# Kernel optimization log

Hardware: AMD Instinct MI355X
Metric: run time of the kernel (lower is better)

## Reference

```python
import jax, jax.numpy as jnp
import numpy as np

B, S, D = 2, 2048, 1024
H = 16
DK = D // H  # 64


def _rope_tables():
    # standard RoPE frequencies, shaped (1,1,S,DK//2) for clean broadcasting
    half = DK // 2
    inv_freq = 1.0 / (10000.0 ** (np.arange(0, half, dtype=np.float32) * 2.0 / DK))
    t = np.arange(S, dtype=np.float32)
    ang = np.einsum('s,d->sd', t, inv_freq)  # (S, half)
    sin = jnp.asarray(np.sin(ang))[None, None]  # (1,1,S,half)
    cos = jnp.asarray(np.cos(ang))[None, None]
    return sin, cos


def setup_inputs() -> dict:
    key = jax.random.key(0)
    ks = jax.random.split(key, 12)
    scale = 1.0 / np.sqrt(D)
    k = jax.random.normal(ks[0], (B, S, D), jnp.float32)
    q = jax.random.normal(ks[1], (B, S, D), jnp.float32)
    v = jax.random.normal(ks[2], (B, S, D), jnp.float32)
    # causal mask, broadcast over batch and heads: (1,1,S,S)
    mask = jnp.tril(jnp.ones((S, S), jnp.int32))[None, None]
    sin, cos = _rope_tables()
    Wk = jax.random.normal(ks[3], (D, D), jnp.float32) * scale
    bk = jax.random.normal(ks[4], (D,), jnp.float32) * scale
    Wq = jax.random.normal(ks[5], (D, D), jnp.float32) * scale
    bq = jax.random.normal(ks[6], (D,), jnp.float32) * scale
    Wv = jax.random.normal(ks[7], (D, D), jnp.float32) * scale
    bv = jax.random.normal(ks[8], (D,), jnp.float32) * scale
    Wo = jax.random.normal(ks[9], (D, D), jnp.float32) * scale
    bo = jax.random.normal(ks[10], (D,), jnp.float32) * scale
    return dict(k=k, q=q, v=v, mask=mask, sin=sin, cos=cos,
                Wk=Wk, bk=bk, Wq=Wq, bq=bq, Wv=Wv, bv=bv, Wo=Wo, bo=bo)


def _apply_rope(x, sin, cos):
    # x: (B,H,S,DK); sin/cos: (1,1,S,DK//2)
    x1 = x[..., ::2]
    x2 = x[..., 1::2]
    even = x1 * cos - x2 * sin
    odd = x1 * sin + x2 * cos
    return jnp.stack((even, odd), axis=-1).reshape(x.shape)


def reference(k, q, v, mask, sin, cos, Wk, bk, Wq, bq, Wv, bv, Wo, bo):
    # projections (nn.Linear: x @ W.T + b)
    def proj(x, W, b):
        y = x @ W.T + b
        return y.reshape(B, S, H, DK).transpose(0, 2, 1, 3)  # (B,H,S,DK)

    key = proj(k, Wk, bk)
    query = proj(q, Wq, bq)
    value = proj(v, Wv, bv)

    query = _apply_rope(query, sin, cos)
    key = _apply_rope(key, sin, cos)

    scores = jnp.einsum('bhqd,bhkd->bhqk', query, key) / jnp.sqrt(jnp.float32(DK))
    scores = jnp.where(mask == 0, jnp.float32(-1e9), scores)
    attn = jax.nn.softmax(scores, axis=-1)  # dropout=0 -> identity
    x = jnp.einsum('bhqk,bhkd->bhqd', attn, value)
    x = x.transpose(0, 2, 1, 3).reshape(B, S, D)
    return x @ Wo.T + bo
```

## Files before the change

### kernel.cpp

```cpp
#include <hip/hip_runtime.h>
#include <hip/hip_bf16.h>

typedef __bf16 bf16x8 __attribute__((ext_vector_type(8)));
typedef __bf16 bf16x4 __attribute__((ext_vector_type(4)));
typedef float  f32x4  __attribute__((ext_vector_type(4)));

static constexpr int B = 2, S = 2048, D = 1024, H = 16, DK = 64;
static constexpr int M = B * S;
static constexpr int NE = M * D;
static constexpr int WE = D * D;

__device__ inline float fast_exp2(float x) { return __builtin_amdgcn_exp2f(x); }

__device__ inline void gload16(const void* g, void* l) {
  __builtin_amdgcn_global_load_lds(
      (const __attribute__((address_space(1))) void*)g,
      (__attribute__((address_space(3))) void*)l, 16, 0, 0);
}

__device__ inline int perm64(int i) {
  return (((i >> 2) & 3) << 4) | (((i >> 5) & 1) << 3) | (((i >> 4) & 1) << 2) | (i & 3);
}

__global__ __launch_bounds__(256) void cvt_all(
    const float* __restrict__ q, const float* __restrict__ k,
    const float* __restrict__ v, const float* __restrict__ Wq,
    const float* __restrict__ Wk, const float* __restrict__ Wv,
    const float* __restrict__ Wo,
    __bf16* __restrict__ Xq, __bf16* __restrict__ Xk,
    __bf16* __restrict__ Xv, __bf16* __restrict__ Wall)
{
  int z = blockIdx.y;
  const float* src; __bf16* dst; int n4;
  switch (z) {
    case 0: src = q;  dst = Xq;            n4 = NE / 4; break;
    case 1: src = k;  dst = Xk;            n4 = NE / 4; break;
    case 2: src = v;  dst = Xv;            n4 = NE / 4; break;
    case 3: src = Wq; dst = Wall;          n4 = WE / 4; break;
    case 4: src = Wk; dst = Wall + WE;     n4 = WE / 4; break;
    case 5: src = Wv; dst = Wall + 2*WE;   n4 = WE / 4; break;
    default:src = Wo; dst = Wall + 3*WE;   n4 = WE / 4; break;
  }
  int i = blockIdx.x * blockDim.x + threadIdx.x;
  int stride = gridDim.x * blockDim.x;
  for (; i < n4; i += stride) {
    float4 f = reinterpret_cast<const float4*>(src)[i];
    bf16x4 o;
    o[0] = (__bf16)f.x; o[1] = (__bf16)f.y; o[2] = (__bf16)f.z; o[3] = (__bf16)f.w;
    reinterpret_cast<bf16x4*>(dst)[i] = o;
  }
}

__global__ __launch_bounds__(256) void proj_kernel(
    const __bf16* __restrict__ Xq, const __bf16* __restrict__ Xk,
    const __bf16* __restrict__ Xv, const __bf16* __restrict__ Wall,
    const float* __restrict__ bq_, const float* __restrict__ bk_,
    const float* __restrict__ bv_,
    const float* __restrict__ sinp, const float* __restrict__ cosp,
    __bf16* __restrict__ Qr, __bf16* __restrict__ Kr, __bf16* __restrict__ Vt)
{
  __shared__ __align__(16) __bf16 As[128 * 32];
  __shared__ __align__(16) __bf16 Bs[128 * 32];
  int tid = threadIdx.x;
  int lane = tid & 63, wid = tid >> 6;
  int lr = lane & 15, lg = lane >> 4;
  int wr = wid >> 1, wc = wid & 1;
  int m0 = blockIdx.x * 128;
  int by = blockIdx.y;
  int z  = by >> 3;
  const __bf16* A    = (z == 0) ? Xq : (z == 1) ? Xk : Xv;
  const __bf16* Bw   = Wall + (size_t)by * 128 * 1024;
  const float*  bias = (z == 0) ? bq_ : (z == 1) ? bk_ : bv_;

  int off0 = tid * 16;
  int row0 = off0 >> 6;
  int ce0  = (off0 & 63) >> 1;
  char* asw = (char*)As + wid * 1024;
  char* bsw = (char*)Bs + wid * 1024;

  f32x4 acc[4][4];
#pragma unroll
  for (int i = 0; i < 4; ++i)
#pragma unroll
    for (int j = 0; j < 4; ++j) acc[i][j] = (f32x4){0, 0, 0, 0};

  for (int k0 = 0; k0 < 1024; k0 += 32) {
    gload16(A  + (size_t)(m0 + row0)      * 1024 + k0 + ce0, asw);
    gload16(A  + (size_t)(m0 + row0 + 64) * 1024 + k0 + ce0, asw + 4096);
    gload16(Bw + (size_t)(row0)           * 1024 + k0 + ce0, bsw);
    gload16(Bw + (size_t)(row0 + 64)      * 1024 + k0 + ce0, bsw + 4096);
    __syncthreads();
    bf16x8 af[4], bf[4];
#pragma unroll
    for (int mi = 0; mi < 4; ++mi)
      af[mi] = *reinterpret_cast<const bf16x8*>(&As[(wr*64 + mi*16 + lr)*32 + lg*8]);
#pragma unroll
    for (int ni = 0; ni < 4; ++ni)
      bf[ni] = *reinterpret_cast<const bf16x8*>(&Bs[(wc*64 + ni*16 + lr)*32 + lg*8]);
#pragma unroll
    for (int mi = 0; mi < 4; ++mi)
#pragma unroll
      for (int ni = 0; ni < 4; ++ni)
        acc[mi][ni] = __builtin_amdgcn_mfma_f32_16x16x32_bf16(af[mi], bf[ni], acc[mi][ni], 0, 0, 0);
    __syncthreads();
  }

#pragma unroll
  for (int ni = 0; ni < 4; ++ni) {
    int cf  = by * 128 + wc * 64 + ni * 16 + lr;
    int col = cf & 1023;
    int h = col >> 6, dk = col & 63, tt = dk >> 1;
    float bval = bias[col];
#pragma unroll
    for (int mi = 0; mi < 4; ++mi) {
#pragma unroll
      for (int i = 0; i < 4; ++i) {
        int r = m0 + wr * 64 + mi * 16 + lg * 4 + i;
        int s = r & (S - 1), bb = r >> 11;
        float val = acc[mi][ni][i] + bval;
        if (z < 2) {
          float part = __shfl_xor(val, 1);
          float sn = sinp[s * 32 + tt], cs = cosp[s * 32 + tt];
          float ov = (dk & 1) ? (part * sn + val * cs) : (val * cs - part * sn);
          if (z == 0) ov *= 0.18033688011112042f;
          __bf16* dst = (z == 0) ? Qr : Kr;
          dst[((size_t)(bb * H + h) * S + s) * DK + dk] = (__bf16)ov;
        } else {
          int sp = (s & ~63) | perm64(s & 63);
          Vt[((size_t)(bb * H + h) * DK + dk) * S + sp] = (__bf16)val;
        }
      }
    }
  }
}

__global__ __launch_bounds__(256) void outproj_kernel(
    const __bf16* __restrict__ AO, const __bf16* __restrict__ Wo,
    const float* __restrict__ bo_, float* __restrict__ out)
{
  __shared__ __align__(16) __bf16 As[128 * 32];
  __shared__ __align__(16) __bf16 Bs[128 * 32];
  int tid = threadIdx.x;
  int lane = tid & 63, wid = tid >> 6;
  int lr = lane & 15, lg = lane >> 4;
  int wr = wid >> 1, wc = wid & 1;
  int m0 = blockIdx.x * 128;
  int n0 = blockIdx.y * 128;

  int off0 = tid * 16;
  int row0 = off0 >> 6;
  int ce0  = (off0 & 63) >> 1;
  char* asw = (char*)As + wid * 1024;
  char* bsw = (char*)Bs + wid * 1024;

  f32x4 acc[4][4];
#pragma unroll
  for (int i = 0; i < 4; ++i)
#pragma unroll
    for (int j = 0; j < 4; ++j) acc[i][j] = (f32x4){0, 0, 0, 0};

  for (int k0 = 0; k0 < 1024; k0 += 32) {
    gload16(AO + (size_t)(m0 + row0)      * 1024 + k0 + ce0, asw);
    gload16(AO + (size_t)(m0 + row0 + 64) * 1024 + k0 + ce0, asw + 4096);
    gload16(Wo + (size_t)(n0 + row0)      * 1024 + k0 + ce0, bsw);
    gload16(Wo + (size_t)(n0 + row0 + 64) * 1024 + k0 + ce0, bsw + 4096);
    __syncthreads();
    bf16x8 af[4], bf[4];
#pragma unroll
    for (int mi = 0; mi < 4; ++mi)
      af[mi] = *reinterpret_cast<const bf16x8*>(&As[(wr*64 + mi*16 + lr)*32 + lg*8]);
#pragma unroll
    for (int ni = 0; ni < 4; ++ni)
      bf[ni] = *reinterpret_cast<const bf16x8*>(&Bs[(wc*64 + ni*16 + lr)*32 + lg*8]);
#pragma unroll
    for (int mi = 0; mi < 4; ++mi)
#pragma unroll
      for (int ni = 0; ni < 4; ++ni)
        acc[mi][ni] = __builtin_amdgcn_mfma_f32_16x16x32_bf16(af[mi], bf[ni], acc[mi][ni], 0, 0, 0);
    __syncthreads();
  }

#pragma unroll
  for (int ni = 0; ni < 4; ++ni) {
    int c = n0 + wc * 64 + ni * 16 + lr;
    float bval = bo_[c];
#pragma unroll
    for (int mi = 0; mi < 4; ++mi)
#pragma unroll
      for (int i = 0; i < 4; ++i) {
        int r = m0 + wr * 64 + mi * 16 + lg * 4 + i;
        out[(size_t)r * 1024 + c] = acc[mi][ni][i] + bval;
      }
  }
}

__global__ __launch_bounds__(256, 4) void attn_kernel(
    const __bf16* __restrict__ Qr, const __bf16* __restrict__ Kr,
    const __bf16* __restrict__ Vt, __bf16* __restrict__ AO)
{
  __shared__ __align__(16) char smem[32768];
  int tid = threadIdx.x;
  int lane = tid & 63, wid = tid >> 6;
  int lr = lane & 15, lg = lane >> 4;
  int bx = blockIdx.x;
  int bh = (bx & 7) * 4 + ((bx >> 3) & 3);
  int qb = 31 - (bx >> 5);
  int q0 = qb * 64 + wid * 16;
  int nsteps = qb + 1;

  const char* Kb = (const char*)(Kr + (size_t)bh * S * DK);
  const char* Vb = (const char*)(Vt + (size_t)bh * DK * S);
  const __bf16* Qh = Qr + (size_t)bh * S * DK;

  int o_lo = wid * 1024 + lane * 16;
#define STAGE(sel, kv0)                                                        \
  {                                                                            \
    char* kdst = smem + (sel) * 16384;                                         \
    _Pragma("unroll")                                                          \
    for (int i = 0; i < 2; ++i) {                                              \
      int o = o_lo + i * 4096;                                                 \
      int row = o >> 7;                                                        \
      int colp = (o & 127) ^ ((row & 7) << 4);                                 \
      gload16(Kb + (((size_t)((kv0) + row)) << 7) + colp,                      \
              kdst + wid * 1024 + i * 4096);                                   \
      gload16(Vb + ((size_t)row * S + (kv0)) * 2 + colp,                       \
              kdst + 8192 + wid * 1024 + i * 4096);                            \
    }                                                                          \
  }

  bf16x8 bq[2];
#pragma unroll
  for (int kc = 0; kc < 2; ++kc)
    bq[kc] = *(const bf16x8*)(Qh + (size_t)(q0 + lr) * DK + kc * 32 + lg * 8);

  int swz = (lr & 7) << 4;
  int oK0 = lr * 128 + ((lg * 16) ^ swz);
  int oK1 = lr * 128 + ((64 + lg * 16) ^ swz);
  int oV0 = lr * 128 + ((lg * 32) ^ swz);
  int oV1 = lr * 128 + ((16 + lg * 32) ^ swz);

  f32x4 o[4];
  float m2 = -3e38f, l2 = 0.f;
#pragma unroll
  for (int dt = 0; dt < 4; ++dt) o[dt] = (f32x4){0, 0, 0, 0};

  STAGE(0, 0);
  __syncthreads();

  for (int j = 0; j < nsteps; ++j) {
    int sel = j & 1;
    if (j + 1 < nsteps) STAGE(sel ^ 1, (j + 1) * 64);
    const char* kbuf = smem + sel * 16384;
    const char* vbuf = kbuf + 8192;
    int kv0 = j * 64;

    f32x4 sc[4];
#pragma unroll
    for (int kt = 0; kt < 4; ++kt) {
      bf16x8 ka0 = *(const bf16x8*)(kbuf + oK0 + kt * 2048);
      bf16x8 ka1 = *(const bf16x8*)(kbuf + oK1 + kt * 2048);
      f32x4 s = (f32x4){0, 0, 0, 0};
      s = __builtin_amdgcn_mfma_f32_16x16x32_bf16(ka0, bq[0], s, 0, 0, 0);
      s = __builtin_amdgcn_mfma_f32_16x16x32_bf16(ka1, bq[1], s, 0, 0, 0);
      sc[kt] = s;
    }

    if (j == qb) {
#pragma unroll
      for (int kt = 0; kt < 4; ++kt)
#pragma unroll
        for (int i = 0; i < 4; ++i)
          if (kv0 + kt * 16 + lg * 4 + i > q0 + lr)
            sc[kt][i] = -3e38f;
    }

    float tm = fmaxf(
        fmaxf(fmaxf(fmaxf(sc[0][0], sc[0][1]), fmaxf(sc[0][2], sc[0][3])),
              fmaxf(fmaxf(sc[1][0], sc[1][1]), fmaxf(sc[1][2], sc[1][3]))),
        fmaxf(fmaxf(fmaxf(sc[2][0], sc[2][1]), fmaxf(sc[2][2], sc[2][3])),
              fmaxf(fmaxf(sc[3][0], sc[3][1]), fmaxf(sc[3][2], sc[3][3]))));
    tm = fmaxf(tm, __shfl_xor(tm, 16));
    tm = fmaxf(tm, __shfl_xor(tm, 32));
    if (__any(tm > m2 + 8.0f)) {
      float mn = fmaxf(m2, tm);
      float f = fast_exp2(m2 - mn);
      m2 = mn;
      l2 *= f;
#pragma unroll
      for (int dt = 0; dt < 4; ++dt) o[dt] *= f;
    }
    float p[16];
#pragma unroll
    for (int kt = 0; kt < 4; ++kt)
#pragma unroll
      for (int i = 0; i < 4; ++i)
        p[kt * 4 + i] = fast_exp2(sc[kt][i] - m2);
    float sum = (((p[0] + p[1]) + (p[2] + p[3])) + ((p[4] + p[5]) + (p[6] + p[7]))) +
                (((p[8] + p[9]) + (p[10] + p[11])) + ((p[12] + p[13]) + (p[14] + p[15])));
    sum += __shfl_xor(sum, 16);
    sum += __shfl_xor(sum, 32);
    l2 += sum;
    bf16x8 pb[2];
#pragma unroll
    for (int kc = 0; kc < 2; ++kc) {
      bf16x8 pv;
#pragma unroll
      for (int a = 0; a < 2; ++a)
#pragma unroll
        for (int r = 0; r < 4; ++r)
          pv[a * 4 + r] = (__bf16)p[(2 * kc + a) * 4 + r];
      pb[kc] = pv;
    }

#pragma unroll
    for (int dt = 0; dt < 4; ++dt) {
      bf16x8 v0 = *(const bf16x8*)(vbuf + oV0 + dt * 2048);
      bf16x8 v1 = *(const bf16x8*)(vbuf + oV1 + dt * 2048);
      o[dt] = __builtin_amdgcn_mfma_f32_16x16x32_bf16(v0, pb[0], o[dt], 0, 0, 0);
      o[dt] = __builtin_amdgcn_mfma_f32_16x16x32_bf16(v1, pb[1], o[dt], 0, 0, 0);
    }
    __syncthreads();
  }
#undef STAGE

  int b = bh >> 4, h = bh & 15;
  float inv = 1.f / l2;
  int s = q0 + lr;
#pragma unroll
  for (int dt = 0; dt < 4; ++dt) {
    bf16x4 w;
#pragma unroll
    for (int i = 0; i < 4; ++i) w[i] = (__bf16)(o[dt][i] * inv);
    *(bf16x4*)&AO[(((size_t)(b * S + s)) * H + h) * DK + dt * 16 + lg * 4] = w;
  }
}

extern "C" void kernel_launch(void* const* d_in, const int* in_sizes, int n_in,
                              void* d_out, int out_size, void* d_ws, size_t ws_size,
                              hipStream_t stream) {
  const float* k_in = (const float*)d_in[0];
  const float* q_in = (const float*)d_in[1];
  const float* v_in = (const float*)d_in[2];
  const float* sinp = (const float*)d_in[4];
  const float* cosp = (const float*)d_in[5];
  const float* Wk = (const float*)d_in[6];
  const float* bk = (const float*)d_in[7];
  const float* Wq = (const float*)d_in[8];
  const float* bq = (const float*)d_in[9];
  const float* Wv = (const float*)d_in[10];
  const float* bv = (const float*)d_in[11];
  const float* Wo = (const float*)d_in[12];
  const float* bo = (const float*)d_in[13];
  float* out = (float*)d_out;

  __bf16* ws   = (__bf16*)d_ws;
  __bf16* Xq   = ws;
  __bf16* Xk   = ws + NE;
  __bf16* Xv   = ws + 2 * NE;
  __bf16* Wall = ws + 3 * NE;
  __bf16* Qr   = ws + 3 * NE + 4 * WE;
  __bf16* Kr   = Qr + NE;
  __bf16* Vt   = Kr + NE;
  __bf16* AO   = Vt + NE;

  dim3 blk(256);
  cvt_all<<<dim3(512, 7), blk, 0, stream>>>(q_in, k_in, v_in, Wq, Wk, Wv, Wo,
                                            Xq, Xk, Xv, Wall);
  proj_kernel<<<dim3(32, 24), blk, 0, stream>>>(Xq, Xk, Xv, Wall, bq, bk, bv,
                                                sinp, cosp, Qr, Kr, Vt);
  attn_kernel<<<1024, blk, 0, stream>>>(Qr, Kr, Vt, AO);
  outproj_kernel<<<dim3(32, 8), blk, 0, stream>>>(AO, Wall + 3 * WE, bo, out);
}
```

Before: 126.5 us.

## Fuse activation fp32-to-bf16 conversion into projection GEMM and transpose output tiles

Removes the separate conversion pass for q/k/v activations. The projection kernel now reads fp32 activations directly from global memory into registers, converts them to bf16 and uses them as MFMA operands, while only the weight tile is staged in LDS. The MFMA operands are swapped so each lane holds four consecutive output columns, which allows vectorized bias loads, paired RoPE math without shuffles, and bf16x4 and float4 stores in both the projection and output projection kernels. The risk is that the activation reads are uncached fp32 loads with no LDS reuse, so each activation row is fetched once per wave column and more global traffic goes into the GEMM loop.

```diff
diff --git a/kernel.cpp b/kernel.cpp
--- a/kernel.cpp
+++ b/kernel.cpp
@@ -22,25 +22,15 @@
   return (((i >> 2) & 3) << 4) | (((i >> 5) & 1) << 3) | (((i >> 4) & 1) << 2) | (i & 3);
 }
 
-__global__ __launch_bounds__(256) void cvt_all(
-    const float* __restrict__ q, const float* __restrict__ k,
-    const float* __restrict__ v, const float* __restrict__ Wq,
-    const float* __restrict__ Wk, const float* __restrict__ Wv,
-    const float* __restrict__ Wo,
-    __bf16* __restrict__ Xq, __bf16* __restrict__ Xk,
-    __bf16* __restrict__ Xv, __bf16* __restrict__ Wall)
+__global__ __launch_bounds__(256) void cvt_w(
+    const float* __restrict__ Wq, const float* __restrict__ Wk,
+    const float* __restrict__ Wv, const float* __restrict__ Wo,
+    __bf16* __restrict__ Wall)
 {
   int z = blockIdx.y;
-  const float* src; __bf16* dst; int n4;
-  switch (z) {
-    case 0: src = q;  dst = Xq;            n4 = NE / 4; break;
-    case 1: src = k;  dst = Xk;            n4 = NE / 4; break;
-    case 2: src = v;  dst = Xv;            n4 = NE / 4; break;
-    case 3: src = Wq; dst = Wall;          n4 = WE / 4; break;
-    case 4: src = Wk; dst = Wall + WE;     n4 = WE / 4; break;
-    case 5: src = Wv; dst = Wall + 2*WE;   n4 = WE / 4; break;
-    default:src = Wo; dst = Wall + 3*WE;   n4 = WE / 4; break;
-  }
+  const float* src = (z == 0) ? Wq : (z == 1) ? Wk : (z == 2) ? Wv : Wo;
+  __bf16* dst = Wall + (size_t)z * WE;
+  int n4 = WE / 4;
   int i = blockIdx.x * blockDim.x + threadIdx.x;
   int stride = gridDim.x * blockDim.x;
   for (; i < n4; i += stride) {
@@ -52,15 +42,14 @@
 }
 
 __global__ __launch_bounds__(256) void proj_kernel(
-    const __bf16* __restrict__ Xq, const __bf16* __restrict__ Xk,
-    const __bf16* __restrict__ Xv, const __bf16* __restrict__ Wall,
+    const float* __restrict__ Xq32, const float* __restrict__ Xk32,
+    const float* __restrict__ Xv32, const __bf16* __restrict__ Wall,
     const float* __restrict__ bq_, const float* __restrict__ bk_,
     const float* __restrict__ bv_,
     const float* __restrict__ sinp, const float* __restrict__ cosp,
     __bf16* __restrict__ Qr, __bf16* __restrict__ Kr, __bf16* __restrict__ Vt)
 {
-  __shared__ __align__(16) __bf16 As[128 * 32];
-  __shared__ __align__(16) __bf16 Bs[128 * 32];
+  __shared__ __align__(16) __bf16 Ws[128 * 32];
   int tid = threadIdx.x;
   int lane = tid & 63, wid = tid >> 6;
   int lr = lane & 15, lg = lane >> 4;
@@ -68,15 +57,18 @@
   int m0 = blockIdx.x * 128;
   int by = blockIdx.y;
   int z  = by >> 3;
-  const __bf16* A    = (z == 0) ? Xq : (z == 1) ? Xk : Xv;
+  const float*  X32  = (z == 0) ? Xq32 : (z == 1) ? Xk32 : Xv32;
   const __bf16* Bw   = Wall + (size_t)by * 128 * 1024;
   const float*  bias = (z == 0) ? bq_ : (z == 1) ? bk_ : bv_;
 
-  int off0 = tid * 16;
-  int row0 = off0 >> 6;
-  int ce0  = (off0 & 63) >> 1;
-  char* asw = (char*)As + wid * 1024;
-  char* bsw = (char*)Bs + wid * 1024;
+  int row0 = tid >> 2;
+  int ce0  = (tid & 3) * 8;
+  char* bsw = (char*)Ws + wid * 1024;
+
+  const float* xbase[4];
+#pragma unroll
+  for (int ni = 0; ni < 4; ++ni)
+    xbase[ni] = X32 + (size_t)(m0 + wc * 64 + ni * 16 + lr) * 1024 + lg * 8;
 
   f32x4 acc[4][4];
 #pragma unroll
@@ -85,50 +77,65 @@
     for (int j = 0; j < 4; ++j) acc[i][j] = (f32x4){0, 0, 0, 0};
 
   for (int k0 = 0; k0 < 1024; k0 += 32) {
-    gload16(A  + (size_t)(m0 + row0)      * 1024 + k0 + ce0, asw);
-    gload16(A  + (size_t)(m0 + row0 + 64) * 1024 + k0 + ce0, asw + 4096);
-    gload16(Bw + (size_t)(row0)           * 1024 + k0 + ce0, bsw);
-    gload16(Bw + (size_t)(row0 + 64)      * 1024 + k0 + ce0, bsw + 4096);
-    __syncthreads();
-    bf16x8 af[4], bf[4];
+    gload16(Bw + (size_t)row0 * 1024 + k0 + ce0, bsw);
+    gload16(Bw + (size_t)(row0 + 64) * 1024 + k0 + ce0, bsw + 4096);
+    bf16x8 bfr[4];
+#pragma unroll
+    for (int ni = 0; ni < 4; ++ni) {
+      float4 xa = *reinterpret_cast<const float4*>(xbase[ni] + k0);
+      float4 xb = *reinterpret_cast<const float4*>(xbase[ni] + k0 + 4);
+      bf16x8 v;
+      v[0] = (__bf16)xa.x; v[1] = (__bf16)xa.y; v[2] = (__bf16)xa.z; v[3] = (__bf16)xa.w;
+      v[4] = (__bf16)xb.x; v[5] = (__bf16)xb.y; v[6] = (__bf16)xb.z; v[7] = (__bf16)xb.w;
+      bfr[ni] = v;
+    }
+    __syncthreads();
+    bf16x8 af[4];
 #pragma unroll
     for (int mi = 0; mi < 4; ++mi)
-      af[mi] = *reinterpret_cast<const bf16x8*>(&As[(wr*64 + mi*16 + lr)*32 + lg*8]);
-#pragma unroll
-    for (int ni = 0; ni < 4; ++ni)
-      bf[ni] = *reinterpret_cast<const bf16x8*>(&Bs[(wc*64 + ni*16 + lr)*32 + lg*8]);
+      af[mi] = *reinterpret_cast<const bf16x8*>(&Ws[(wr*64 + mi*16 + lr)*32 + lg*8]);
 #pragma unroll
     for (int mi = 0; mi < 4; ++mi)
 #pragma unroll
       for (int ni = 0; ni < 4; ++ni)
-        acc[mi][ni] = __builtin_amdgcn_mfma_f32_16x16x32_bf16(af[mi], bf[ni], acc[mi][ni], 0, 0, 0);
-    __syncthreads();
-  }
-
-#pragma unroll
-  for (int ni = 0; ni < 4; ++ni) {
-    int cf  = by * 128 + wc * 64 + ni * 16 + lr;
-    int col = cf & 1023;
-    int h = col >> 6, dk = col & 63, tt = dk >> 1;
-    float bval = bias[col];
-#pragma unroll
-    for (int mi = 0; mi < 4; ++mi) {
-#pragma unroll
-      for (int i = 0; i < 4; ++i) {
-        int r = m0 + wr * 64 + mi * 16 + lg * 4 + i;
-        int s = r & (S - 1), bb = r >> 11;
-        float val = acc[mi][ni][i] + bval;
-        if (z < 2) {
-          float part = __shfl_xor(val, 1);
-          float sn = sinp[s * 32 + tt], cs = cosp[s * 32 + tt];
-          float ov = (dk & 1) ? (part * sn + val * cs) : (val * cs - part * sn);
-          if (z == 0) ov *= 0.18033688011112042f;
-          __bf16* dst = (z == 0) ? Qr : Kr;
-          dst[((size_t)(bb * H + h) * S + s) * DK + dk] = (__bf16)ov;
-        } else {
-          int sp = (s & ~63) | perm64(s & 63);
-          Vt[((size_t)(bb * H + h) * DK + dk) * S + sp] = (__bf16)val;
+        acc[mi][ni] = __builtin_amdgcn_mfma_f32_16x16x32_bf16(af[mi], bfr[ni], acc[mi][ni], 0, 0, 0);
+    __syncthreads();
+  }
+
+#pragma unroll
+  for (int mi = 0; mi < 4; ++mi) {
+    int dkf0 = by * 128 + wr * 64 + mi * 16 + lg * 4;
+    int col0 = dkf0 & 1023;
+    int h = col0 >> 6, dk0 = col0 & 63, t0 = dk0 >> 1;
+    float4 bv4 = *reinterpret_cast<const float4*>(&bias[col0]);
+#pragma unroll
+    for (int ni = 0; ni < 4; ++ni) {
+      int r = m0 + wc * 64 + ni * 16 + lr;
+      int s = r & (S - 1), bb = r >> 11;
+      float v0 = acc[mi][ni][0] + bv4.x;
+      float v1 = acc[mi][ni][1] + bv4.y;
+      float v2 = acc[mi][ni][2] + bv4.z;
+      float v3 = acc[mi][ni][3] + bv4.w;
+      if (z < 2) {
+        float2 sn = *reinterpret_cast<const float2*>(&sinp[s * 32 + t0]);
+        float2 cs = *reinterpret_cast<const float2*>(&cosp[s * 32 + t0]);
+        float e0 = v0 * cs.x - v1 * sn.x, o0 = v0 * sn.x + v1 * cs.x;
+        float e1 = v2 * cs.y - v3 * sn.y, o1 = v2 * sn.y + v3 * cs.y;
+        if (z == 0) {
+          e0 *= 0.18033688011112042f; o0 *= 0.18033688011112042f;
+          e1 *= 0.18033688011112042f; o1 *= 0.18033688011112042f;
         }
+        bf16x4 w;
+        w[0] = (__bf16)e0; w[1] = (__bf16)o0; w[2] = (__bf16)e1; w[3] = (__bf16)o1;
+        __bf16* dst = (z == 0) ? Qr : Kr;
+        *(bf16x4*)&dst[((size_t)(bb * H + h) * S + s) * DK + dk0] = w;
+      } else {
+        int sp = (s & ~63) | perm64(s & 63);
+        size_t base = ((size_t)(bb * H + h) * DK + dk0) * S + sp;
+        Vt[base]         = (__bf16)v0;
+        Vt[base + S]     = (__bf16)v1;
+        Vt[base + 2 * S] = (__bf16)v2;
+        Vt[base + 3 * S] = (__bf16)v3;
       }
     }
   }
@@ -147,9 +154,8 @@
   int m0 = blockIdx.x * 128;
   int n0 = blockIdx.y * 128;
 
-  int off0 = tid * 16;
-  int row0 = off0 >> 6;
-  int ce0  = (off0 & 63) >> 1;
+  int row0 = tid >> 2;
+  int ce0  = (tid & 3) * 8;
   char* asw = (char*)As + wid * 1024;
   char* bsw = (char*)Bs + wid * 1024;
 
@@ -165,32 +171,35 @@
     gload16(Wo + (size_t)(n0 + row0)      * 1024 + k0 + ce0, bsw);
     gload16(Wo + (size_t)(n0 + row0 + 64) * 1024 + k0 + ce0, bsw + 4096);
     __syncthreads();
-    bf16x8 af[4], bf[4];
+    bf16x8 wf[4], aof[4];
 #pragma unroll
     for (int mi = 0; mi < 4; ++mi)
-      af[mi] = *reinterpret_cast<const bf16x8*>(&As[(wr*64 + mi*16 + lr)*32 + lg*8]);
+      wf[mi]  = *reinterpret_cast<const bf16x8*>(&Bs[(wr*64 + mi*16 + lr)*32 + lg*8]);
 #pragma unroll
     for (int ni = 0; ni < 4; ++ni)
-      bf[ni] = *reinterpret_cast<const bf16x8*>(&Bs[(wc*64 + ni*16 + lr)*32 + lg*8]);
+      aof[ni] = *reinterpret_cast<const bf16x8*>(&As[(wc*64 + ni*16 + lr)*32 + lg*8]);
 #pragma unroll
     for (int mi = 0; mi < 4; ++mi)
 #pragma unroll
       for (int ni = 0; ni < 4; ++ni)
-        acc[mi][ni] = __builtin_amdgcn_mfma_f32_16x16x32_bf16(af[mi], bf[ni], acc[mi][ni], 0, 0, 0);
-    __syncthreads();
-  }
-
-#pragma unroll
-  for (int ni = 0; ni < 4; ++ni) {
-    int c = n0 + wc * 64 + ni * 16 + lr;
-    float bval = bo_[c];
-#pragma unroll
-    for (int mi = 0; mi < 4; ++mi)
-#pragma unroll
-      for (int i = 0; i < 4; ++i) {
-        int r = m0 + wr * 64 + mi * 16 + lg * 4 + i;
-        out[(size_t)r * 1024 + c] = acc[mi][ni][i] + bval;
-      }
+        acc[mi][ni] = __builtin_amdgcn_mfma_f32_16x16x32_bf16(wf[mi], aof[ni], acc[mi][ni], 0, 0, 0);
+    __syncthreads();
+  }
+
+#pragma unroll
+  for (int mi = 0; mi < 4; ++mi) {
+    int c0 = n0 + wr * 64 + mi * 16 + lg * 4;
+    float4 bv4 = *reinterpret_cast<const float4*>(&bo_[c0]);
+#pragma unroll
+    for (int ni = 0; ni < 4; ++ni) {
+      int r = m0 + wc * 64 + ni * 16 + lr;
+      float4 w;
+      w.x = acc[mi][ni][0] + bv4.x;
+      w.y = acc[mi][ni][1] + bv4.y;
+      w.z = acc[mi][ni][2] + bv4.z;
+      w.w = acc[mi][ni][3] + bv4.w;
+      *reinterpret_cast<float4*>(&out[(size_t)r * 1024 + c0]) = w;
+    }
   }
 }
 
@@ -354,19 +363,15 @@
   float* out = (float*)d_out;
 
   __bf16* ws   = (__bf16*)d_ws;
-  __bf16* Xq   = ws;
-  __bf16* Xk   = ws + NE;
-  __bf16* Xv   = ws + 2 * NE;
-  __bf16* Wall = ws + 3 * NE;
-  __bf16* Qr   = ws + 3 * NE + 4 * WE;
+  __bf16* Wall = ws;
+  __bf16* Qr   = ws + 4 * WE;
   __bf16* Kr   = Qr + NE;
   __bf16* Vt   = Kr + NE;
   __bf16* AO   = Vt + NE;
 
   dim3 blk(256);
-  cvt_all<<<dim3(512, 7), blk, 0, stream>>>(q_in, k_in, v_in, Wq, Wk, Wv, Wo,
-                                            Xq, Xk, Xv, Wall);
-  proj_kernel<<<dim3(32, 24), blk, 0, stream>>>(Xq, Xk, Xv, Wall, bq, bk, bv,
+  cvt_w<<<dim3(512, 4), blk, 0, stream>>>(Wq, Wk, Wv, Wo, Wall);
+  proj_kernel<<<dim3(32, 24), blk, 0, stream>>>(q_in, k_in, v_in, Wall, bq, bk, bv,
                                                 sinp, cosp, Qr, Kr, Vt);
   attn_kernel<<<1024, blk, 0, stream>>>(Qr, Kr, Vt, AO);
   outproj_kernel<<<dim3(32, 8), blk, 0, stream>>>(AO, Wall + 3 * WE, bo, out);
```

After: 177.6 us. 40.4% more time.
